# Performance work log

Hardware: AMD Instinct MI355X
Metric: run time of the kernel (lower is better)

## Reference

```python
import jax, jax.numpy as jnp
import numpy as np
from jax import lax

B, L, D, K = 4, 4096, 2048, 4
EPS = 1e-5


def setup_inputs() -> dict:
    key = jax.random.key(0)
    k1, k2, k3 = jax.random.split(key, 3)
    x = jax.random.normal(k1, (B, L, D), dtype=jnp.float32)
    # RMSNorm learned scale (torch nn.RMSNorm weight), perturbed around 1
    norm_weight = 1.0 + 0.02 * jax.random.normal(k2, (D,), dtype=jnp.float32)
    # depthwise conv weight in jax 'WIO' layout: (K, 1, D). torch layout is (D, 1, K).
    conv_weight = 0.1 * jax.random.normal(k3, (K, 1, D), dtype=jnp.float32)
    return {"x": x, "norm_weight": norm_weight, "conv_weight": conv_weight}


def reference(x, norm_weight, conv_weight):
    # RMSNorm over last dim: x / sqrt(mean(x^2) + eps) * weight
    ms = jnp.mean(jnp.square(x), axis=-1, keepdims=True)
    x_norm = x * lax.rsqrt(ms + EPS) * norm_weight  # (B, L, D)

    # Depthwise causal conv1d: left-pad K-1 zeros along L (equivalent to
    # torch's symmetric padding=(K-1) followed by [..., :L] slice).
    y = lax.conv_general_dilated(
        x_norm,                     # (B, L, D)
        conv_weight,                # (K, 1, D)
        window_strides=(1,),
        padding=[(K - 1, 0)],
        dimension_numbers=("NWC", "WIO", "NWC"),
        feature_group_count=D,
    )                               # (B, L, D)

    # SiLU activation
    return y * jax.nn.sigmoid(y)
```

## Files before the change

### kernel.cpp

```cpp
#include <hip/hip_runtime.h>

constexpr int B = 4;
constexpr int L = 4096;
constexpr int D = 2048;
constexpr int K = 4;
constexpr float EPS = 1e-5f;

constexpr int CL = 16;
constexpr int NW = 8;

__device__ __forceinline__ void load4(const float* p, float r[4]) {
    float4 v = *reinterpret_cast<const float4*>(p);
    r[0] = v.x; r[1] = v.y; r[2] = v.z; r[3] = v.w;
}

__device__ __forceinline__ float row_invrms(float s, float* slot, int wave, int lane) {
    #pragma unroll
    for (int off = 32; off > 0; off >>= 1)
        s += __shfl_down(s, off, 64);
    if (lane == 0) slot[wave] = s;
    __syncthreads();
    float tot = 0.0f;
    #pragma unroll
    for (int w = 0; w < NW; ++w) tot += slot[w];
    return rsqrtf(tot * (1.0f / D) + EPS);
}

__global__ __launch_bounds__(512) void fused_kernel(const float* __restrict__ x,
                                                    const float* __restrict__ nw,
                                                    const float* __restrict__ cw,
                                                    float* __restrict__ out) {
    const int t = threadIdx.x;
    const int wave = t >> 6;
    const int lane = t & 63;
    const int chunk = blockIdx.x;
    const int b = blockIdx.y;
    const int l0 = chunk * CL;
    const int d = t * 4;

    const float* xb = x + (size_t)b * L * D;
    float* ob = out + (size_t)b * L * D;

    __shared__ float s_red[2][NW];
    int par = 0;

    float nwv[4], w0v[4], w1v[4], w2v[4], w3v[4];
    load4(nw + d, nwv);
    load4(cw + 0 * D + d, w0v);
    load4(cw + 1 * D + d, w1v);
    load4(cw + 2 * D + d, w2v);
    load4(cw + 3 * D + d, w3v);

    float win[3][4];
    #pragma unroll
    for (int j = 0; j < 3; ++j) {
        const int l = l0 - 3 + j;
        float xv[4] = {0.f, 0.f, 0.f, 0.f};
        if (l >= 0) load4(xb + (size_t)l * D + d, xv);
        float s = xv[0]*xv[0] + xv[1]*xv[1] + xv[2]*xv[2] + xv[3]*xv[3];
        float irms = row_invrms(s, s_red[par], wave, lane);
        par ^= 1;
        #pragma unroll
        for (int i = 0; i < 4; ++i) win[j][i] = xv[i] * irms * nwv[i];
    }

    float xnext[4];
    load4(xb + (size_t)l0 * D + d, xnext);

    for (int li = 0; li < CL; ++li) {
        float xv[4];
        #pragma unroll
        for (int i = 0; i < 4; ++i) xv[i] = xnext[i];
        if (li + 1 < CL)
            load4(xb + (size_t)(l0 + li + 1) * D + d, xnext);

        float s = xv[0]*xv[0] + xv[1]*xv[1] + xv[2]*xv[2] + xv[3]*xv[3];
        float irms = row_invrms(s, s_red[par], wave, lane);
        par ^= 1;

        float cur[4], y[4];
        #pragma unroll
        for (int i = 0; i < 4; ++i) {
            cur[i] = xv[i] * irms * nwv[i];
            y[i] = w0v[i] * win[0][i] + w1v[i] * win[1][i]
                 + w2v[i] * win[2][i] + w3v[i] * cur[i];
            float sg = 1.0f / (1.0f + __expf(-y[i]));
            y[i] *= sg;
        }

        *reinterpret_cast<float4*>(ob + (size_t)(l0 + li) * D + d) =
            make_float4(y[0], y[1], y[2], y[3]);

        #pragma unroll
        for (int i = 0; i < 4; ++i) {
            win[0][i] = win[1][i];
            win[1][i] = win[2][i];
            win[2][i] = cur[i];
        }
    }
}

extern "C" void kernel_launch(void* const* d_in, const int* in_sizes, int n_in,
                              void* d_out, int out_size, void* d_ws, size_t ws_size,
                              hipStream_t stream) {
    const float* x  = (const float*)d_in[0];
    const float* nw = (const float*)d_in[1];
    const float* cw = (const float*)d_in[2];
    float* out = (float*)d_out;

    fused_kernel<<<dim3(L / CL, B), 512, 0, stream>>>(x, nw, cw, out);
}
```

Baseline: 51.52 us.

## Batch row RMS reductions four at a time and prefetch row groups

Processes rows in groups of four, so the four row reductions share a single block barrier instead of one barrier per row. The three halo rows also share one barrier. The next group of four rows is loaded before the barrier, giving deeper prefetch, and outputs now use nontemporal stores. This cuts barrier count and exposed load latency at the cost of more registers per thread.

```diff
diff --git a/kernel.cpp b/kernel.cpp
--- a/kernel.cpp
+++ b/kernel.cpp
@@ -3,27 +3,18 @@
 constexpr int B = 4;
 constexpr int L = 4096;
 constexpr int D = 2048;
-constexpr int K = 4;
 constexpr float EPS = 1e-5f;
 
 constexpr int CL = 16;
+constexpr int R  = 4;
+constexpr int NG = CL / R;
 constexpr int NW = 8;
 
-__device__ __forceinline__ void load4(const float* p, float r[4]) {
-    float4 v = *reinterpret_cast<const float4*>(p);
+typedef float floatx4 __attribute__((ext_vector_type(4)));
+
+__device__ __forceinline__ void load4(const float* __restrict__ p, float r[4]) {
+    floatx4 v = *reinterpret_cast<const floatx4*>(p);
     r[0] = v.x; r[1] = v.y; r[2] = v.z; r[3] = v.w;
-}
-
-__device__ __forceinline__ float row_invrms(float s, float* slot, int wave, int lane) {
-    #pragma unroll
-    for (int off = 32; off > 0; off >>= 1)
-        s += __shfl_down(s, off, 64);
-    if (lane == 0) slot[wave] = s;
-    __syncthreads();
-    float tot = 0.0f;
-    #pragma unroll
-    for (int w = 0; w < NW; ++w) tot += slot[w];
-    return rsqrtf(tot * (1.0f / D) + EPS);
 }
 
 __global__ __launch_bounds__(512) void fused_kernel(const float* __restrict__ x,
@@ -33,70 +24,106 @@
     const int t = threadIdx.x;
     const int wave = t >> 6;
     const int lane = t & 63;
-    const int chunk = blockIdx.x;
+    const int l0 = blockIdx.x * CL;
     const int b = blockIdx.y;
-    const int l0 = chunk * CL;
     const int d = t * 4;
 
-    const float* xb = x + (size_t)b * L * D;
-    float* ob = out + (size_t)b * L * D;
+    const float* xb = x + (size_t)b * L * D + d;
+    float* ob = out + (size_t)b * L * D + d;
 
-    __shared__ float s_red[2][NW];
-    int par = 0;
+    __shared__ float s_red[2][R][NW];
 
-    float nwv[4], w0v[4], w1v[4], w2v[4], w3v[4];
+    float nwv[4], wv[4][4];
     load4(nw + d, nwv);
-    load4(cw + 0 * D + d, w0v);
-    load4(cw + 1 * D + d, w1v);
-    load4(cw + 2 * D + d, w2v);
-    load4(cw + 3 * D + d, w3v);
+    #pragma unroll
+    for (int k = 0; k < 4; ++k) load4(cw + k * D + d, wv[k]);
 
     float win[3][4];
-    #pragma unroll
-    for (int j = 0; j < 3; ++j) {
-        const int l = l0 - 3 + j;
-        float xv[4] = {0.f, 0.f, 0.f, 0.f};
-        if (l >= 0) load4(xb + (size_t)l * D + d, xv);
-        float s = xv[0]*xv[0] + xv[1]*xv[1] + xv[2]*xv[2] + xv[3]*xv[3];
-        float irms = row_invrms(s, s_red[par], wave, lane);
-        par ^= 1;
+    {
+        float hx[3][4];
         #pragma unroll
-        for (int i = 0; i < 4; ++i) win[j][i] = xv[i] * irms * nwv[i];
+        for (int j = 0; j < 3; ++j) {
+            const int l = l0 - 3 + j;
+            hx[j][0] = hx[j][1] = hx[j][2] = hx[j][3] = 0.0f;
+            if (l >= 0) load4(xb + (size_t)l * D, hx[j]);
+            float s = hx[j][0]*hx[j][0] + hx[j][1]*hx[j][1]
+                    + hx[j][2]*hx[j][2] + hx[j][3]*hx[j][3];
+            #pragma unroll
+            for (int off = 32; off > 0; off >>= 1)
+                s += __shfl_down(s, off, 64);
+            if (lane == 0) s_red[0][j][wave] = s;
+        }
+        __syncthreads();
+        #pragma unroll
+        for (int j = 0; j < 3; ++j) {
+            float tot = 0.0f;
+            #pragma unroll
+            for (int w = 0; w < NW; ++w) tot += s_red[0][j][w];
+            float irms = rsqrtf(tot * (1.0f / D) + EPS);
+            #pragma unroll
+            for (int i = 0; i < 4; ++i) win[j][i] = hx[j][i] * irms * nwv[i];
+        }
     }
 
-    float xnext[4];
-    load4(xb + (size_t)l0 * D + d, xnext);
+    float cur[R][4], nxt[R][4];
+    #pragma unroll
+    for (int r = 0; r < R; ++r)
+        load4(xb + (size_t)(l0 + r) * D, cur[r]);
 
-    for (int li = 0; li < CL; ++li) {
-        float xv[4];
+    #pragma unroll
+    for (int g = 0; g < NG; ++g) {
+        const int par = (g + 1) & 1;
+
         #pragma unroll
-        for (int i = 0; i < 4; ++i) xv[i] = xnext[i];
-        if (li + 1 < CL)
-            load4(xb + (size_t)(l0 + li + 1) * D + d, xnext);
-
-        float s = xv[0]*xv[0] + xv[1]*xv[1] + xv[2]*xv[2] + xv[3]*xv[3];
-        float irms = row_invrms(s, s_red[par], wave, lane);
-        par ^= 1;
-
-        float cur[4], y[4];
-        #pragma unroll
-        for (int i = 0; i < 4; ++i) {
-            cur[i] = xv[i] * irms * nwv[i];
-            y[i] = w0v[i] * win[0][i] + w1v[i] * win[1][i]
-                 + w2v[i] * win[2][i] + w3v[i] * cur[i];
-            float sg = 1.0f / (1.0f + __expf(-y[i]));
-            y[i] *= sg;
+        for (int r = 0; r < R; ++r) {
+            float s = cur[r][0]*cur[r][0] + cur[r][1]*cur[r][1]
+                    + cur[r][2]*cur[r][2] + cur[r][3]*cur[r][3];
+            #pragma unroll
+            for (int off = 32; off > 0; off >>= 1)
+                s += __shfl_down(s, off, 64);
+            if (lane == 0) s_red[par][r][wave] = s;
         }
 
-        *reinterpret_cast<float4*>(ob + (size_t)(l0 + li) * D + d) =
-            make_float4(y[0], y[1], y[2], y[3]);
+        if (g + 1 < NG) {
+            #pragma unroll
+            for (int r = 0; r < R; ++r)
+                load4(xb + (size_t)(l0 + (g + 1) * R + r) * D, nxt[r]);
+        }
+
+        __syncthreads();
 
         #pragma unroll
-        for (int i = 0; i < 4; ++i) {
-            win[0][i] = win[1][i];
-            win[1][i] = win[2][i];
-            win[2][i] = cur[i];
+        for (int r = 0; r < R; ++r) {
+            float tot = 0.0f;
+            #pragma unroll
+            for (int w = 0; w < NW; ++w) tot += s_red[par][r][w];
+            const float irms = rsqrtf(tot * (1.0f / D) + EPS);
+
+            float c[4], y[4];
+            #pragma unroll
+            for (int i = 0; i < 4; ++i) {
+                c[i] = cur[r][i] * irms * nwv[i];
+                y[i] = wv[0][i]*win[0][i] + wv[1][i]*win[1][i]
+                     + wv[2][i]*win[2][i] + wv[3][i]*c[i];
+                y[i] = y[i] / (1.0f + __expf(-y[i]));
+            }
+            floatx4 o;
+            o.x = y[0]; o.y = y[1]; o.z = y[2]; o.w = y[3];
+            __builtin_nontemporal_store(o,
+                reinterpret_cast<floatx4*>(ob + (size_t)(l0 + g * R + r) * D));
+
+            #pragma unroll
+            for (int i = 0; i < 4; ++i) {
+                win[0][i] = win[1][i];
+                win[1][i] = win[2][i];
+                win[2][i] = c[i];
+            }
         }
+
+        #pragma unroll
+        for (int r = 0; r < R; ++r)
+            #pragma unroll
+            for (int i = 0; i < 4; ++i) cur[r][i] = nxt[r][i];
     }
 }
 
```

New measurement: 50.51 us. 2.0% less time.

## Batch all row RMS reductions behind a single barrier with register-held rows

Applied to the files above, without the earlier changes.

The kernel now loads all 19 rows (16 outputs plus 3 halo rows) into registers up front, does every wave-level reduction, and uses a single __syncthreads instead of one barrier per row. Norm weights are folded into the conv weights, the block index is swizzled across XCDs, and output stores are nontemporal. The cost targeted is the 19 serialized barriers and the load latency exposed one row at a time. In exchange, register pressure rises (76 floats of row data), with launch_bounds asking for 4 blocks per CU.

```diff
diff --git a/kernel.cpp b/kernel.cpp
--- a/kernel.cpp
+++ b/kernel.cpp
@@ -3,100 +3,86 @@
 constexpr int B = 4;
 constexpr int L = 4096;
 constexpr int D = 2048;
-constexpr int K = 4;
 constexpr float EPS = 1e-5f;
 
 constexpr int CL = 16;
+constexpr int NR = CL + 3;
 constexpr int NW = 8;
+constexpr int NCHUNK = L / CL;
+constexpr int NWG = NCHUNK * B;
 
-__device__ __forceinline__ void load4(const float* p, float r[4]) {
-    float4 v = *reinterpret_cast<const float4*>(p);
-    r[0] = v.x; r[1] = v.y; r[2] = v.z; r[3] = v.w;
-}
+typedef float floatx4 __attribute__((ext_vector_type(4)));
 
-__device__ __forceinline__ float row_invrms(float s, float* slot, int wave, int lane) {
-    #pragma unroll
-    for (int off = 32; off > 0; off >>= 1)
-        s += __shfl_down(s, off, 64);
-    if (lane == 0) slot[wave] = s;
-    __syncthreads();
-    float tot = 0.0f;
-    #pragma unroll
-    for (int w = 0; w < NW; ++w) tot += slot[w];
-    return rsqrtf(tot * (1.0f / D) + EPS);
-}
-
-__global__ __launch_bounds__(512) void fused_kernel(const float* __restrict__ x,
-                                                    const float* __restrict__ nw,
-                                                    const float* __restrict__ cw,
-                                                    float* __restrict__ out) {
+__global__ __launch_bounds__(512, 4) void fused_kernel(const float* __restrict__ x,
+                                                       const float* __restrict__ nw,
+                                                       const float* __restrict__ cw,
+                                                       float* __restrict__ out) {
     const int t = threadIdx.x;
     const int wave = t >> 6;
     const int lane = t & 63;
-    const int chunk = blockIdx.x;
-    const int b = blockIdx.y;
+
+    const int bid = blockIdx.x;
+    const int swz = (bid & 7) * (NWG / 8) + (bid >> 3);
+    const int b = swz / NCHUNK;
+    const int chunk = swz % NCHUNK;
     const int l0 = chunk * CL;
     const int d = t * 4;
 
-    const float* xb = x + (size_t)b * L * D;
-    float* ob = out + (size_t)b * L * D;
+    const float* xb = x + (size_t)b * L * D + d;
+    float* ob = out + (size_t)b * L * D + d;
 
-    __shared__ float s_red[2][NW];
-    int par = 0;
+    __shared__ __align__(16) float s_red[NR][NW];
 
-    float nwv[4], w0v[4], w1v[4], w2v[4], w3v[4];
-    load4(nw + d, nwv);
-    load4(cw + 0 * D + d, w0v);
-    load4(cw + 1 * D + d, w1v);
-    load4(cw + 2 * D + d, w2v);
-    load4(cw + 3 * D + d, w3v);
+    const floatx4 nwv = *reinterpret_cast<const floatx4*>(nw + d);
+    floatx4 wn[4];
+    #pragma unroll
+    for (int k = 0; k < 4; ++k)
+        wn[k] = *reinterpret_cast<const floatx4*>(cw + k * D + d) * nwv;
 
-    float win[3][4];
+    floatx4 hx[NR];
     #pragma unroll
-    for (int j = 0; j < 3; ++j) {
+    for (int j = 0; j < NR; ++j) {
         const int l = l0 - 3 + j;
-        float xv[4] = {0.f, 0.f, 0.f, 0.f};
-        if (l >= 0) load4(xb + (size_t)l * D + d, xv);
-        float s = xv[0]*xv[0] + xv[1]*xv[1] + xv[2]*xv[2] + xv[3]*xv[3];
-        float irms = row_invrms(s, s_red[par], wave, lane);
-        par ^= 1;
-        #pragma unroll
-        for (int i = 0; i < 4; ++i) win[j][i] = xv[i] * irms * nwv[i];
+        if (l >= 0)
+            hx[j] = *reinterpret_cast<const floatx4*>(xb + (size_t)l * D);
+        else
+            hx[j] = (floatx4)0.0f;
     }
 
-    float xnext[4];
-    load4(xb + (size_t)l0 * D + d, xnext);
+    #pragma unroll
+    for (int j = 0; j < NR; ++j) {
+        float s = hx[j].x * hx[j].x + hx[j].y * hx[j].y
+                + hx[j].z * hx[j].z + hx[j].w * hx[j].w;
+        #pragma unroll
+        for (int off = 32; off > 0; off >>= 1)
+            s += __shfl_down(s, off, 64);
+        if (lane == 0) s_red[j][wave] = s;
+    }
 
+    __syncthreads();
+
+    #pragma unroll
+    for (int j = 0; j < NR; ++j) {
+        floatx4 p0 = *reinterpret_cast<const floatx4*>(&s_red[j][0]);
+        floatx4 p1 = *reinterpret_cast<const floatx4*>(&s_red[j][4]);
+        float tot = ((p0.x + p0.y) + (p0.z + p0.w))
+                  + ((p1.x + p1.y) + (p1.z + p1.w));
+        const float irms = rsqrtf(tot * (1.0f / D) + EPS);
+        hx[j] *= irms;
+    }
+
+    #pragma unroll
     for (int li = 0; li < CL; ++li) {
-        float xv[4];
-        #pragma unroll
-        for (int i = 0; i < 4; ++i) xv[i] = xnext[i];
-        if (li + 1 < CL)
-            load4(xb + (size_t)(l0 + li + 1) * D + d, xnext);
-
-        float s = xv[0]*xv[0] + xv[1]*xv[1] + xv[2]*xv[2] + xv[3]*xv[3];
-        float irms = row_invrms(s, s_red[par], wave, lane);
-        par ^= 1;
-
-        float cur[4], y[4];
-        #pragma unroll
-        for (int i = 0; i < 4; ++i) {
-            cur[i] = xv[i] * irms * nwv[i];
-            y[i] = w0v[i] * win[0][i] + w1v[i] * win[1][i]
-                 + w2v[i] * win[2][i] + w3v[i] * cur[i];
-            float sg = 1.0f / (1.0f + __expf(-y[i]));
-            y[i] *= sg;
-        }
-
-        *reinterpret_cast<float4*>(ob + (size_t)(l0 + li) * D + d) =
-            make_float4(y[0], y[1], y[2], y[3]);
-
-        #pragma unroll
-        for (int i = 0; i < 4; ++i) {
-            win[0][i] = win[1][i];
-            win[1][i] = win[2][i];
-            win[2][i] = cur[i];
-        }
+        floatx4 y = wn[0] * hx[li]     + wn[1] * hx[li + 1]
+                  + wn[2] * hx[li + 2] + wn[3] * hx[li + 3];
+        floatx4 sg;
+        sg.x = 1.0f / (1.0f + __expf(-y.x));
+        sg.y = 1.0f / (1.0f + __expf(-y.y));
+        sg.z = 1.0f / (1.0f + __expf(-y.z));
+        sg.w = 1.0f / (1.0f + __expf(-y.w));
+        y *= sg;
+        __builtin_nontemporal_store(y,
+            reinterpret_cast<floatx4*>(ob + (size_t)(l0 + li) * D));
     }
 }
 
@@ -108,5 +94,5 @@
     const float* cw = (const float*)d_in[2];
     float* out = (float*)d_out;
 
-    fused_kernel<<<dim3(L / CL, B), 512, 0, stream>>>(x, nw, cw, out);
+    fused_kernel<<<NWG, 512, 0, stream>>>(x, nw, cw, out);
 }
```

Result: slower. 52.88 us (+2.6%).
